# Performance work log

Hardware: AMD Instinct MI355X
Metric: run time of the kernel (lower is better)

## Reference

```python
import jax, jax.numpy as jnp
import numpy as np

DIM = 1024
N_HEADS = 16
HEAD_DIM = DIM // N_HEADS
SCALE = HEAD_DIM ** -0.5


def setup_inputs() -> dict:
    key = jax.random.key(0)
    ks = jax.random.split(key, 10)
    B, L, L_low = 4, 4096, 1024
    s = DIM ** -0.5
    return {
        "x_broad": jax.random.normal(ks[0], (B, L, DIM), jnp.float32),
        "x_low": jax.random.normal(ks[1], (B, L_low, DIM), jnp.float32),
        "Wq": jax.random.normal(ks[2], (DIM, DIM), jnp.float32) * s,
        "bq": jnp.zeros((DIM,), jnp.float32),
        "Wk": jax.random.normal(ks[3], (DIM, DIM), jnp.float32) * s,
        "bk": jnp.zeros((DIM,), jnp.float32),
        "Wv": jax.random.normal(ks[4], (DIM, DIM), jnp.float32) * s,
        "bv": jnp.zeros((DIM,), jnp.float32),
        "Wo": jax.random.normal(ks[5], (DIM, DIM), jnp.float32) * s,
        "bo": jnp.zeros((DIM,), jnp.float32),
    }


def reference(x_broad, x_low, Wq, bq, Wk, bk, Wv, bv, Wo, bo):
    B, L, D = x_broad.shape
    Ll = x_low.shape[1]
    # projections (torch Linear: x @ W.T + b)
    q = (x_broad @ Wq.T + bq).reshape(B, L, N_HEADS, HEAD_DIM)
    k = (x_low @ Wk.T + bk).reshape(B, Ll, N_HEADS, HEAD_DIM)
    v = (x_low @ Wv.T + bv).reshape(B, Ll, N_HEADS, HEAD_DIM)
    # scores: [B, H, L, L_low]
    attn = jnp.einsum("blhd,bmhd->bhlm", q, k) * SCALE
    attn = jax.nn.softmax(attn, axis=-1)
    out = jnp.einsum("bhlm,bmhd->blhd", attn, v).reshape(B, L, D)
    return out @ Wo.T + bo
```

## Files before the change

kernel.cpp:

```cpp
#include <hip/hip_runtime.h>
#include <hip/hip_bf16.h>

typedef __bf16 bf16;
typedef __bf16 bf16x4 __attribute__((ext_vector_type(4)));
typedef __bf16 bf16x8 __attribute__((ext_vector_type(8)));
typedef float f32x4 __attribute__((ext_vector_type(4)));

#define MFMA16(a, b, c) __builtin_amdgcn_mfma_f32_16x16x32_bf16(a, b, c, 0, 0, 0)

constexpr int DIM = 1024;
constexpr int NH = 16;
constexpr int HD = 64;
constexpr float SCALE = 0.125f;
constexpr float L2E = 1.4426950408889634f;
constexpr float SCL2E = SCALE * L2E;

__device__ __forceinline__ float fast_exp2(float x) {
  float r;
  asm("v_exp_f32 %0, %1" : "=v"(r) : "v"(x));
  return r;
}

__device__ __forceinline__ void gl_lds16(const void* g, void* l) {
  __builtin_amdgcn_global_load_lds((const __attribute__((address_space(1))) void*)g,
                                   (__attribute__((address_space(3))) void*)l, 16, 0, 0);
}

__global__ __launch_bounds__(256) void cvt_f32_bf16(const float* __restrict__ s,
                                                    bf16* __restrict__ d, int n8) {
  const int i = blockIdx.x * 256 + threadIdx.x;
  if (i < n8) {
    const float4 v0 = ((const float4*)s)[i * 2];
    const float4 v1 = ((const float4*)s)[i * 2 + 1];
    bf16x8 o = {(bf16)v0.x, (bf16)v0.y, (bf16)v0.z, (bf16)v0.w,
                (bf16)v1.x, (bf16)v1.y, (bf16)v1.z, (bf16)v1.w};
    ((bf16x8*)d)[i] = o;
  }
}

__global__ __launch_bounds__(256) void cvt_w4(const float* __restrict__ a,
                                              const float* __restrict__ b,
                                              const float* __restrict__ c,
                                              const float* __restrict__ d,
                                              bf16* __restrict__ o) {
  constexpr int N8 = DIM * DIM / 8;
  const int i = blockIdx.x * 256 + threadIdx.x;
  const int g = i >> 17;
  const int j = i & (N8 - 1);
  const float* s = (g == 0) ? a : (g == 1) ? b : (g == 2) ? c : d;
  const float4 v0 = ((const float4*)s)[j * 2];
  const float4 v1 = ((const float4*)s)[j * 2 + 1];
  bf16x8 ov = {(bf16)v0.x, (bf16)v0.y, (bf16)v0.z, (bf16)v0.w,
               (bf16)v1.x, (bf16)v1.y, (bf16)v1.z, (bf16)v1.w};
  ((bf16x8*)o)[i] = ov;
}

template <int OUT_MODE>
__global__ __launch_bounds__(256) void gemm_bf16(const bf16* __restrict__ A,
                                                 const bf16* __restrict__ W,
                                                 const float* __restrict__ bias,
                                                 void* __restrict__ Cptr, int Lq,
                                                 float oscale) {
  __shared__ bf16 As[128 * 64];
  __shared__ bf16 Bs[128 * 64];

  const int bm = blockIdx.x * 128;
  const int bn = blockIdx.y * 128;
  const int tid = threadIdx.x;
  const int w = tid >> 6;
  const int lane = tid & 63;
  const int quad = lane >> 4;
  const int l16 = lane & 15;
  const int wm = (w >> 1) * 64;
  const int wn = (w & 1) * 64;
  const int lr = lane >> 3;
  const int sc8 = (((lane & 7) ^ lr)) << 3;
  const int x7 = l16 & 7;

  size_t aOff[4], bOff[4];
#pragma unroll
  for (int r = 0; r < 4; ++r) {
    const int rowt = (r * 4 + w) * 8 + lr;
    aOff[r] = (size_t)(bm + rowt) * DIM + sc8;
    bOff[r] = (size_t)(bn + rowt) * DIM + sc8;
  }

  f32x4 acc[4][4] = {};

  for (int k0 = 0; k0 < DIM; k0 += 64) {
#pragma unroll
    for (int r = 0; r < 4; ++r) {
      gl_lds16(A + aOff[r] + k0, (char*)As + (r * 4 + w) * 1024);
      gl_lds16(W + bOff[r] + k0, (char*)Bs + (r * 4 + w) * 1024);
    }
    __syncthreads();

#pragma unroll
    for (int s = 0; s < 2; ++s) {
      bf16x8 af[4], bfr[4];
#pragma unroll
      for (int mi = 0; mi < 4; ++mi)
        af[mi] = *(const bf16x8*)((char*)As + (wm + mi * 16 + l16) * 128 +
                                  (((quad + 4 * s) ^ x7) << 4));
#pragma unroll
      for (int ni = 0; ni < 4; ++ni)
        bfr[ni] = *(const bf16x8*)((char*)Bs + (wn + ni * 16 + l16) * 128 +
                                   (((quad + 4 * s) ^ x7) << 4));
#pragma unroll
      for (int mi = 0; mi < 4; ++mi)
#pragma unroll
        for (int ni = 0; ni < 4; ++ni)
          acc[mi][ni] = MFMA16(af[mi], bfr[ni], acc[mi][ni]);
    }
    __syncthreads();
  }

#pragma unroll
  for (int mi = 0; mi < 4; ++mi) {
#pragma unroll
    for (int ni = 0; ni < 4; ++ni) {
      const int col = bn + wn + ni * 16 + l16;
      const float bv = bias[col];
#pragma unroll
      for (int r = 0; r < 4; ++r) {
        const int row = bm + wm + mi * 16 + quad * 4 + r;
        const float val = (acc[mi][ni][r] + bv) * oscale;
        if constexpr (OUT_MODE == 0) {
          ((float*)Cptr)[(size_t)row * DIM + col] = val;
        } else if constexpr (OUT_MODE == 1) {
          const int b = row / Lq;
          const int l = row - b * Lq;
          ((bf16*)Cptr)[((size_t)((b * NH + (col >> 6)) * Lq + l) << 6) + (col & 63)] =
              (bf16)val;
        } else {
          const int b = row >> 10;
          const int kv = row & 1023;
          ((bf16*)Cptr)[(((size_t)(b * NH + (col >> 6)) << 6) + (col & 63)) * 1024 + kv] =
              (bf16)val;
        }
      }
    }
  }
}

template <int OUT_MODE, bool A_BF16>
__global__ __launch_bounds__(256) void gemm_nt(const void* __restrict__ Aptr,
                                               const float* __restrict__ W,
                                               const float* __restrict__ bias,
                                               void* __restrict__ Cptr, int Lq,
                                               float oscale) {
  constexpr int LDT = 72;
  __shared__ bf16 As[128 * LDT];
  __shared__ bf16 Bs[128 * LDT];

  const int bm = blockIdx.x * 128;
  const int bn = blockIdx.y * 128;
  const int tid = threadIdx.x;
  const int w = tid >> 6;
  const int lane = tid & 63;
  const int quad = lane >> 4;
  const int l16 = lane & 15;
  const int wm = (w >> 1) * 64;
  const int wn = (w & 1) * 64;

  f32x4 acc[4][4] = {};

  for (int k0 = 0; k0 < DIM; k0 += 64) {
#pragma unroll
    for (int i = 0; i < 8; ++i) {
      int f = i * 256 + tid;
      int row = f >> 4;
      int c4 = (f & 15) << 2;
      const float4 v = *(const float4*)(W + (size_t)(bn + row) * DIM + k0 + c4);
      bf16x4 bv = {(bf16)v.x, (bf16)v.y, (bf16)v.z, (bf16)v.w};
      *(bf16x4*)&Bs[row * LDT + c4] = bv;
    }
    if constexpr (A_BF16) {
      const bf16* Ab = (const bf16*)Aptr;
#pragma unroll
      for (int i = 0; i < 4; ++i) {
        int f = i * 256 + tid;
        int row = f >> 3;
        int c8 = (f & 7) << 3;
        *(bf16x8*)&As[row * LDT + c8] =
            *(const bf16x8*)(Ab + (size_t)(bm + row) * DIM + k0 + c8);
      }
    } else {
      const float* Af = (const float*)Aptr;
#pragma unroll
      for (int i = 0; i < 8; ++i) {
        int f = i * 256 + tid;
        int row = f >> 4;
        int c4 = (f & 15) << 2;
        const float4 v = *(const float4*)(Af + (size_t)(bm + row) * DIM + k0 + c4);
        bf16x4 av = {(bf16)v.x, (bf16)v.y, (bf16)v.z, (bf16)v.w};
        *(bf16x4*)&As[row * LDT + c4] = av;
      }
    }
    __syncthreads();

#pragma unroll
    for (int sub = 0; sub < 2; ++sub) {
      bf16x8 af[4], bfr[4];
#pragma unroll
      for (int mi = 0; mi < 4; ++mi)
        af[mi] = *(const bf16x8*)&As[(wm + mi * 16 + l16) * LDT + sub * 32 + quad * 8];
#pragma unroll
      for (int ni = 0; ni < 4; ++ni)
        bfr[ni] = *(const bf16x8*)&Bs[(wn + ni * 16 + l16) * LDT + sub * 32 + quad * 8];
#pragma unroll
      for (int mi = 0; mi < 4; ++mi)
#pragma unroll
        for (int ni = 0; ni < 4; ++ni)
          acc[mi][ni] = MFMA16(af[mi], bfr[ni], acc[mi][ni]);
    }
    __syncthreads();
  }

#pragma unroll
  for (int mi = 0; mi < 4; ++mi) {
#pragma unroll
    for (int ni = 0; ni < 4; ++ni) {
      const int col = bn + wn + ni * 16 + l16;
      const float bv = bias[col];
#pragma unroll
      for (int r = 0; r < 4; ++r) {
        const int row = bm + wm + mi * 16 + quad * 4 + r;
        const float val = (acc[mi][ni][r] + bv) * oscale;
        if constexpr (OUT_MODE == 0) {
          ((float*)Cptr)[(size_t)row * DIM + col] = val;
        } else if constexpr (OUT_MODE == 1) {
          const int b = row / Lq;
          const int l = row - b * Lq;
          ((bf16*)Cptr)[((size_t)((b * NH + (col >> 6)) * Lq + l) << 6) + (col & 63)] =
              (bf16)val;
        } else {
          const int b = row >> 10;
          const int kv = row & 1023;
          ((bf16*)Cptr)[(((size_t)(b * NH + (col >> 6)) << 6) + (col & 63)) * 1024 + kv] =
              (bf16)val;
        }
      }
    }
  }
}

__global__ __launch_bounds__(256) void attn_fused(const bf16* __restrict__ Q,
                                                  const bf16* __restrict__ K,
                                                  const bf16* __restrict__ VT,
                                                  bf16* __restrict__ O) {
  __shared__ bf16 Ks[2][64 * 64];
  __shared__ bf16 Vs[2][64 * 64];
  __shared__ bf16 Ps[4 * 16 * 64];

  const int qt = blockIdx.x;
  const int h = blockIdx.y;
  const int b = blockIdx.z;
  const int tid = threadIdx.x;
  const int w = tid >> 6;
  const int lane = tid & 63;
  const int quad = lane >> 4;
  const int l16 = lane & 15;
  const int lr = lane >> 3;
  const int sc8 = (((lane & 7) ^ lr)) << 3;
  const int x7 = l16 & 7;

  const bf16* Qp = Q + ((size_t)(b * NH + h) * 4096 + qt * 128 + w * 32 + l16) * HD + quad * 8;
  const bf16* Kb = K + (size_t)(b * NH + h) * 1024 * HD;
  const bf16* Vb = VT + (size_t)(b * NH + h) * HD * 1024;

  bf16x8 qf[2][2];
#pragma unroll
  for (int g = 0; g < 2; ++g)
#pragma unroll
    for (int s = 0; s < 2; ++s) qf[g][s] = *(const bf16x8*)(Qp + g * 16 * HD + s * 32);

  char* pw = (char*)&Ps[w * 16 * 64];

  f32x4 oacc[2][4] = {};
  f32x4 lacc[2] = {};

  bf16x8 ones;
#pragma unroll
  for (int i = 0; i < 8; ++i) ones[i] = (bf16)1.0f;

  auto stage = [&](int kt, int bi) {
#pragma unroll
    for (int c2 = 0; c2 < 2; ++c2) {
      const int c = c2 * 4 + w;
      gl_lds16(Kb + (size_t)(kt + c * 8 + lr) * HD + sc8, (char*)&Ks[bi][0] + c * 1024);
      gl_lds16(Vb + (size_t)(c * 8 + lr) * 1024 + kt + sc8, (char*)&Vs[bi][0] + c * 1024);
    }
  };

  stage(0, 0);
  int buf = 0;
  for (int kt = 0; kt < 1024; kt += 64) {
    __syncthreads();
    if (kt + 64 < 1024) stage(kt + 64, buf ^ 1);

    bf16x8 kf[4][2];
#pragma unroll
    for (int nt = 0; nt < 4; ++nt)
#pragma unroll
      for (int s = 0; s < 2; ++s)
        kf[nt][s] = *(const bf16x8*)((char*)&Ks[buf][0] + (nt * 16 + l16) * 128 +
                                     (((quad + 4 * s) ^ x7) << 4));

    bf16x8 pf[2][2];
#pragma unroll
    for (int g = 0; g < 2; ++g) {
      __builtin_amdgcn_s_setprio(1);
#pragma unroll
      for (int nt = 0; nt < 4; ++nt) {
        f32x4 a = {0.f, 0.f, 0.f, 0.f};
        a = MFMA16(kf[nt][0], qf[g][0], a);
        a = MFMA16(kf[nt][1], qf[g][1], a);
        bf16x4 pb;
#pragma unroll
        for (int r = 0; r < 4; ++r) pb[r] = (bf16)fast_exp2(a[r]);
        *(bf16x4*)(pw + l16 * 128 + ((nt * 32 + quad * 8) ^ (x7 << 4))) = pb;
      }
      __builtin_amdgcn_s_setprio(0);
#pragma unroll
      for (int s = 0; s < 2; ++s)
        pf[g][s] = *(const bf16x8*)(pw + l16 * 128 + ((s * 64 + quad * 16) ^ (x7 << 4)));
      lacc[g] = MFMA16(ones, pf[g][0], lacc[g]);
      lacc[g] = MFMA16(ones, pf[g][1], lacc[g]);
    }

    __builtin_amdgcn_s_setprio(1);
#pragma unroll
    for (int dt = 0; dt < 4; ++dt) {
      bf16x8 vf0 = *(const bf16x8*)((char*)&Vs[buf][0] + (dt * 16 + l16) * 128 +
                                    ((quad ^ x7) << 4));
      bf16x8 vf1 = *(const bf16x8*)((char*)&Vs[buf][0] + (dt * 16 + l16) * 128 +
                                    ((((quad + 4)) ^ x7) << 4));
      oacc[0][dt] = MFMA16(vf0, pf[0][0], oacc[0][dt]);
      oacc[0][dt] = MFMA16(vf1, pf[0][1], oacc[0][dt]);
      oacc[1][dt] = MFMA16(vf0, pf[1][0], oacc[1][dt]);
      oacc[1][dt] = MFMA16(vf1, pf[1][1], oacc[1][dt]);
    }
    __builtin_amdgcn_s_setprio(0);
    buf ^= 1;
  }

  const float inv[2] = {1.f / lacc[0][0], 1.f / lacc[1][0]};

#pragma unroll
  for (int g = 0; g < 2; ++g) {
    const size_t orow =
        ((size_t)(b * 4096 + qt * 128 + w * 32 + g * 16 + l16)) * DIM + h * 64;
#pragma unroll
    for (int dt = 0; dt < 4; ++dt) {
      bf16x4 ov = {(bf16)(oacc[g][dt][0] * inv[g]), (bf16)(oacc[g][dt][1] * inv[g]),
                   (bf16)(oacc[g][dt][2] * inv[g]), (bf16)(oacc[g][dt][3] * inv[g])};
      *(bf16x4*)(O + orow + dt * 16 + quad * 4) = ov;
    }
  }
}

extern "C" void kernel_launch(void* const* d_in, const int* in_sizes, int n_in,
                              void* d_out, int out_size, void* d_ws, size_t ws_size,
                              hipStream_t stream) {
  const float* x_broad = (const float*)d_in[0];
  const float* x_low = (const float*)d_in[1];
  const float* Wq = (const float*)d_in[2];
  const float* bq = (const float*)d_in[3];
  const float* Wk = (const float*)d_in[4];
  const float* bk = (const float*)d_in[5];
  const float* Wv = (const float*)d_in[6];
  const float* bv = (const float*)d_in[7];
  const float* Wo = (const float*)d_in[8];
  const float* bo = (const float*)d_in[9];

  constexpr int B = 4, L = 4096, LL = 1024;
  const size_t qBytes = (size_t)B * NH * L * HD * 2;
  const size_t kvBytes = (size_t)B * NH * LL * HD * 2;
  const size_t oBytes = qBytes;
  const size_t xlBytes = kvBytes;
  const size_t wBytes = (size_t)DIM * DIM * 2;

  char* ws = (char*)d_ws;
  bf16* Qw = (bf16*)ws;
  bf16* Kw = (bf16*)(ws + qBytes);
  bf16* Vw = (bf16*)(ws + qBytes + kvBytes);
  bf16* Ow = (bf16*)(ws + qBytes + 2 * kvBytes);

  const dim3 blk(256);
  const size_t need = qBytes + 2 * kvBytes + oBytes + xlBytes + 4 * wBytes;

  if (ws_size >= need) {
    bf16* xbB = Ow;
    bf16* xlB = (bf16*)(ws + qBytes + 2 * kvBytes + oBytes);
    bf16* WqB = (bf16*)(ws + qBytes + 2 * kvBytes + oBytes + xlBytes);
    bf16* WkB = WqB + (size_t)DIM * DIM;
    bf16* WvB = WkB + (size_t)DIM * DIM;
    bf16* WoB = WvB + (size_t)DIM * DIM;

    hipLaunchKernelGGL(cvt_f32_bf16, dim3(B * L * DIM / 8 / 256), blk, 0, stream,
                       x_broad, xbB, B * L * DIM / 8);
    hipLaunchKernelGGL(cvt_f32_bf16, dim3(B * LL * DIM / 8 / 256), blk, 0, stream,
                       x_low, xlB, B * LL * DIM / 8);
    hipLaunchKernelGGL(cvt_w4, dim3(4 * DIM * DIM / 8 / 256), blk, 0, stream, Wq, Wk,
                       Wv, Wo, WqB);

    hipLaunchKernelGGL((gemm_bf16<1>), dim3(B * L / 128, DIM / 128), blk, 0, stream,
                       xbB, WqB, bq, Qw, L, SCL2E);
    hipLaunchKernelGGL((gemm_bf16<1>), dim3(B * LL / 128, DIM / 128), blk, 0, stream,
                       xlB, WkB, bk, Kw, LL, 1.0f);
    hipLaunchKernelGGL((gemm_bf16<2>), dim3(B * LL / 128, DIM / 128), blk, 0, stream,
                       xlB, WvB, bv, Vw, LL, 1.0f);
    hipLaunchKernelGGL(attn_fused, dim3(L / 128, NH, B), blk, 0, stream, Qw, Kw, Vw, Ow);
    hipLaunchKernelGGL((gemm_bf16<0>), dim3(B * L / 128, DIM / 128), blk, 0, stream,
                       Ow, WoB, bo, d_out, 1, 1.0f);
  } else {
    hipLaunchKernelGGL((gemm_nt<1, false>), dim3(B * L / 128, DIM / 128), blk, 0,
                       stream, x_broad, Wq, bq, Qw, L, SCL2E);
    hipLaunchKernelGGL((gemm_nt<1, false>), dim3(B * LL / 128, DIM / 128), blk, 0,
                       stream, x_low, Wk, bk, Kw, LL, 1.0f);
    hipLaunchKernelGGL((gemm_nt<2, false>), dim3(B * LL / 128, DIM / 128), blk, 0,
                       stream, x_low, Wv, bv, Vw, LL, 1.0f);
    hipLaunchKernelGGL(attn_fused, dim3(L / 128, NH, B), blk, 0, stream, Qw, Kw, Vw, Ow);
    hipLaunchKernelGGL((gemm_nt<0, true>), dim3(B * L / 128, DIM / 128), blk, 0,
                       stream, Ow, Wo, bo, d_out, 1, 1.0f);
  }
}
```

Measured before the change: 372.5 us.

## Double attention query tile per block and compute V projection transposed

The attention kernel now handles 256 query rows per block (64 per wave, four 16-row groups), so each staged K/V tile is reused across twice as many queries and the grid is halved. The V projection is recomputed as Wv·x_low^T with swapped operands (OUT_MODE 3, per-row bias), so the transposed V layout is written with contiguous kv stores instead of strided scatter. This costs more accumulator registers per wave (lower occupancy possible) and fewer blocks in the attention grid.

```diff
diff --git a/kernel.cpp b/kernel.cpp
--- a/kernel.cpp
+++ b/kernel.cpp
@@ -106,6 +106,109 @@
       for (int ni = 0; ni < 4; ++ni)
         bfr[ni] = *(const bf16x8*)((char*)Bs + (wn + ni * 16 + l16) * 128 +
                                    (((quad + 4 * s) ^ x7) << 4));
+#pragma unroll
+      for (int mi = 0; mi < 4; ++mi)
+#pragma unroll
+        for (int ni = 0; ni < 4; ++ni)
+          acc[mi][ni] = MFMA16(af[mi], bfr[ni], acc[mi][ni]);
+    }
+    __syncthreads();
+  }
+
+#pragma unroll
+  for (int mi = 0; mi < 4; ++mi) {
+#pragma unroll
+    for (int ni = 0; ni < 4; ++ni) {
+      const int col = bn + wn + ni * 16 + l16;
+      const float bv = (OUT_MODE == 3) ? 0.f : bias[col];
+#pragma unroll
+      for (int r = 0; r < 4; ++r) {
+        const int row = bm + wm + mi * 16 + quad * 4 + r;
+        if constexpr (OUT_MODE == 0) {
+          const float val = (acc[mi][ni][r] + bv) * oscale;
+          ((float*)Cptr)[(size_t)row * DIM + col] = val;
+        } else if constexpr (OUT_MODE == 1) {
+          const float val = (acc[mi][ni][r] + bv) * oscale;
+          const int b = row / Lq;
+          const int l = row - b * Lq;
+          ((bf16*)Cptr)[((size_t)((b * NH + (col >> 6)) * Lq + l) << 6) + (col & 63)] =
+              (bf16)val;
+        } else {
+          const float val = acc[mi][ni][r] + bias[row];
+          const int bb = col >> 10;
+          const int kv = col & 1023;
+          ((bf16*)Cptr)[((size_t)(bb * 1024 + row)) * 1024 + kv] = (bf16)val;
+        }
+      }
+    }
+  }
+}
+
+template <int OUT_MODE, bool A_BF16>
+__global__ __launch_bounds__(256) void gemm_nt(const void* __restrict__ Aptr,
+                                               const float* __restrict__ W,
+                                               const float* __restrict__ bias,
+                                               void* __restrict__ Cptr, int Lq,
+                                               float oscale) {
+  constexpr int LDT = 72;
+  __shared__ bf16 As[128 * LDT];
+  __shared__ bf16 Bs[128 * LDT];
+
+  const int bm = blockIdx.x * 128;
+  const int bn = blockIdx.y * 128;
+  const int tid = threadIdx.x;
+  const int w = tid >> 6;
+  const int lane = tid & 63;
+  const int quad = lane >> 4;
+  const int l16 = lane & 15;
+  const int wm = (w >> 1) * 64;
+  const int wn = (w & 1) * 64;
+
+  f32x4 acc[4][4] = {};
+
+  for (int k0 = 0; k0 < DIM; k0 += 64) {
+#pragma unroll
+    for (int i = 0; i < 8; ++i) {
+      int f = i * 256 + tid;
+      int row = f >> 4;
+      int c4 = (f & 15) << 2;
+      const float4 v = *(const float4*)(W + (size_t)(bn + row) * DIM + k0 + c4);
+      bf16x4 bv = {(bf16)v.x, (bf16)v.y, (bf16)v.z, (bf16)v.w};
+      *(bf16x4*)&Bs[row * LDT + c4] = bv;
+    }
+    if constexpr (A_BF16) {
+      const bf16* Ab = (const bf16*)Aptr;
+#pragma unroll
+      for (int i = 0; i < 4; ++i) {
+        int f = i * 256 + tid;
+        int row = f >> 3;
+        int c8 = (f & 7) << 3;
+        *(bf16x8*)&As[row * LDT + c8] =
+            *(const bf16x8*)(Ab + (size_t)(bm + row) * DIM + k0 + c8);
+      }
+    } else {
+      const float* Af = (const float*)Aptr;
+#pragma unroll
+      for (int i = 0; i < 8; ++i) {
+        int f = i * 256 + tid;
+        int row = f >> 4;
+        int c4 = (f & 15) << 2;
+        const float4 v = *(const float4*)(Af + (size_t)(bm + row) * DIM + k0 + c4);
+        bf16x4 av = {(bf16)v.x, (bf16)v.y, (bf16)v.z, (bf16)v.w};
+        *(bf16x4*)&As[row * LDT + c4] = av;
+      }
+    }
+    __syncthreads();
+
+#pragma unroll
+    for (int sub = 0; sub < 2; ++sub) {
+      bf16x8 af[4], bfr[4];
+#pragma unroll
+      for (int mi = 0; mi < 4; ++mi)
+        af[mi] = *(const bf16x8*)&As[(wm + mi * 16 + l16) * LDT + sub * 32 + quad * 8];
+#pragma unroll
+      for (int ni = 0; ni < 4; ++ni)
+        bfr[ni] = *(const bf16x8*)&Bs[(wn + ni * 16 + l16) * LDT + sub * 32 + quad * 8];
 #pragma unroll
       for (int mi = 0; mi < 4; ++mi)
 #pragma unroll
@@ -143,108 +246,6 @@
   }
 }
 
-template <int OUT_MODE, bool A_BF16>
-__global__ __launch_bounds__(256) void gemm_nt(const void* __restrict__ Aptr,
-                                               const float* __restrict__ W,
-                                               const float* __restrict__ bias,
-                                               void* __restrict__ Cptr, int Lq,
-                                               float oscale) {
-  constexpr int LDT = 72;
-  __shared__ bf16 As[128 * LDT];
-  __shared__ bf16 Bs[128 * LDT];
-
-  const int bm = blockIdx.x * 128;
-  const int bn = blockIdx.y * 128;
-  const int tid = threadIdx.x;
-  const int w = tid >> 6;
-  const int lane = tid & 63;
-  const int quad = lane >> 4;
-  const int l16 = lane & 15;
-  const int wm = (w >> 1) * 64;
-  const int wn = (w & 1) * 64;
-
-  f32x4 acc[4][4] = {};
-
-  for (int k0 = 0; k0 < DIM; k0 += 64) {
-#pragma unroll
-    for (int i = 0; i < 8; ++i) {
-      int f = i * 256 + tid;
-      int row = f >> 4;
-      int c4 = (f & 15) << 2;
-      const float4 v = *(const float4*)(W + (size_t)(bn + row) * DIM + k0 + c4);
-      bf16x4 bv = {(bf16)v.x, (bf16)v.y, (bf16)v.z, (bf16)v.w};
-      *(bf16x4*)&Bs[row * LDT + c4] = bv;
-    }
-    if constexpr (A_BF16) {
-      const bf16* Ab = (const bf16*)Aptr;
-#pragma unroll
-      for (int i = 0; i < 4; ++i) {
-        int f = i * 256 + tid;
-        int row = f >> 3;
-        int c8 = (f & 7) << 3;
-        *(bf16x8*)&As[row * LDT + c8] =
-            *(const bf16x8*)(Ab + (size_t)(bm + row) * DIM + k0 + c8);
-      }
-    } else {
-      const float* Af = (const float*)Aptr;
-#pragma unroll
-      for (int i = 0; i < 8; ++i) {
-        int f = i * 256 + tid;
-        int row = f >> 4;
-        int c4 = (f & 15) << 2;
-        const float4 v = *(const float4*)(Af + (size_t)(bm + row) * DIM + k0 + c4);
-        bf16x4 av = {(bf16)v.x, (bf16)v.y, (bf16)v.z, (bf16)v.w};
-        *(bf16x4*)&As[row * LDT + c4] = av;
-      }
-    }
-    __syncthreads();
-
-#pragma unroll
-    for (int sub = 0; sub < 2; ++sub) {
-      bf16x8 af[4], bfr[4];
-#pragma unroll
-      for (int mi = 0; mi < 4; ++mi)
-        af[mi] = *(const bf16x8*)&As[(wm + mi * 16 + l16) * LDT + sub * 32 + quad * 8];
-#pragma unroll
-      for (int ni = 0; ni < 4; ++ni)
-        bfr[ni] = *(const bf16x8*)&Bs[(wn + ni * 16 + l16) * LDT + sub * 32 + quad * 8];
-#pragma unroll
-      for (int mi = 0; mi < 4; ++mi)
-#pragma unroll
-        for (int ni = 0; ni < 4; ++ni)
-          acc[mi][ni] = MFMA16(af[mi], bfr[ni], acc[mi][ni]);
-    }
-    __syncthreads();
-  }
-
-#pragma unroll
-  for (int mi = 0; mi < 4; ++mi) {
-#pragma unroll
-    for (int ni = 0; ni < 4; ++ni) {
-      const int col = bn + wn + ni * 16 + l16;
-      const float bv = bias[col];
-#pragma unroll
-      for (int r = 0; r < 4; ++r) {
-        const int row = bm + wm + mi * 16 + quad * 4 + r;
-        const float val = (acc[mi][ni][r] + bv) * oscale;
-        if constexpr (OUT_MODE == 0) {
-          ((float*)Cptr)[(size_t)row * DIM + col] = val;
-        } else if constexpr (OUT_MODE == 1) {
-          const int b = row / Lq;
-          const int l = row - b * Lq;
-          ((bf16*)Cptr)[((size_t)((b * NH + (col >> 6)) * Lq + l) << 6) + (col & 63)] =
-              (bf16)val;
-        } else {
-          const int b = row >> 10;
-          const int kv = row & 1023;
-          ((bf16*)Cptr)[(((size_t)(b * NH + (col >> 6)) << 6) + (col & 63)) * 1024 + kv] =
-              (bf16)val;
-        }
-      }
-    }
-  }
-}
-
 __global__ __launch_bounds__(256) void attn_fused(const bf16* __restrict__ Q,
                                                   const bf16* __restrict__ K,
                                                   const bf16* __restrict__ VT,
@@ -265,20 +266,21 @@
   const int sc8 = (((lane & 7) ^ lr)) << 3;
   const int x7 = l16 & 7;
 
-  const bf16* Qp = Q + ((size_t)(b * NH + h) * 4096 + qt * 128 + w * 32 + l16) * HD + quad * 8;
+  const bf16* Qp =
+      Q + ((size_t)(b * NH + h) * 4096 + qt * 256 + w * 64 + l16) * HD + quad * 8;
   const bf16* Kb = K + (size_t)(b * NH + h) * 1024 * HD;
   const bf16* Vb = VT + (size_t)(b * NH + h) * HD * 1024;
 
-  bf16x8 qf[2][2];
-#pragma unroll
-  for (int g = 0; g < 2; ++g)
+  bf16x8 qf[4][2];
+#pragma unroll
+  for (int g = 0; g < 4; ++g)
 #pragma unroll
     for (int s = 0; s < 2; ++s) qf[g][s] = *(const bf16x8*)(Qp + g * 16 * HD + s * 32);
 
   char* pw = (char*)&Ps[w * 16 * 64];
 
-  f32x4 oacc[2][4] = {};
-  f32x4 lacc[2] = {};
+  f32x4 oacc[4][4] = {};
+  f32x4 lacc[4] = {};
 
   bf16x8 ones;
 #pragma unroll
@@ -307,9 +309,9 @@
         kf[nt][s] = *(const bf16x8*)((char*)&Ks[buf][0] + (nt * 16 + l16) * 128 +
                                      (((quad + 4 * s) ^ x7) << 4));
 
-    bf16x8 pf[2][2];
-#pragma unroll
-    for (int g = 0; g < 2; ++g) {
+    bf16x8 pf[4][2];
+#pragma unroll
+    for (int g = 0; g < 4; ++g) {
       __builtin_amdgcn_s_setprio(1);
 #pragma unroll
       for (int nt = 0; nt < 4; ++nt) {
@@ -336,25 +338,25 @@
                                     ((quad ^ x7) << 4));
       bf16x8 vf1 = *(const bf16x8*)((char*)&Vs[buf][0] + (dt * 16 + l16) * 128 +
                                     ((((quad + 4)) ^ x7) << 4));
-      oacc[0][dt] = MFMA16(vf0, pf[0][0], oacc[0][dt]);
-      oacc[0][dt] = MFMA16(vf1, pf[0][1], oacc[0][dt]);
-      oacc[1][dt] = MFMA16(vf0, pf[1][0], oacc[1][dt]);
-      oacc[1][dt] = MFMA16(vf1, pf[1][1], oacc[1][dt]);
+#pragma unroll
+      for (int g = 0; g < 4; ++g) {
+        oacc[g][dt] = MFMA16(vf0, pf[g][0], oacc[g][dt]);
+        oacc[g][dt] = MFMA16(vf1, pf[g][1], oacc[g][dt]);
+      }
     }
     __builtin_amdgcn_s_setprio(0);
     buf ^= 1;
   }
 
-  const float inv[2] = {1.f / lacc[0][0], 1.f / lacc[1][0]};
-
-#pragma unroll
-  for (int g = 0; g < 2; ++g) {
+#pragma unroll
+  for (int g = 0; g < 4; ++g) {
+    const float inv = 1.f / lacc[g][0];
     const size_t orow =
-        ((size_t)(b * 4096 + qt * 128 + w * 32 + g * 16 + l16)) * DIM + h * 64;
+        ((size_t)(b * 4096 + qt * 256 + w * 64 + g * 16 + l16)) * DIM + h * 64;
 #pragma unroll
     for (int dt = 0; dt < 4; ++dt) {
-      bf16x4 ov = {(bf16)(oacc[g][dt][0] * inv[g]), (bf16)(oacc[g][dt][1] * inv[g]),
-                   (bf16)(oacc[g][dt][2] * inv[g]), (bf16)(oacc[g][dt][3] * inv[g])};
+      bf16x4 ov = {(bf16)(oacc[g][dt][0] * inv), (bf16)(oacc[g][dt][1] * inv),
+                   (bf16)(oacc[g][dt][2] * inv), (bf16)(oacc[g][dt][3] * inv)};
       *(bf16x4*)(O + orow + dt * 16 + quad * 4) = ov;
     }
   }
@@ -409,9 +411,9 @@
                        xbB, WqB, bq, Qw, L, SCL2E);
     hipLaunchKernelGGL((gemm_bf16<1>), dim3(B * LL / 128, DIM / 128), blk, 0, stream,
                        xlB, WkB, bk, Kw, LL, 1.0f);
-    hipLaunchKernelGGL((gemm_bf16<2>), dim3(B * LL / 128, DIM / 128), blk, 0, stream,
-                       xlB, WvB, bv, Vw, LL, 1.0f);
-    hipLaunchKernelGGL(attn_fused, dim3(L / 128, NH, B), blk, 0, stream, Qw, Kw, Vw, Ow);
+    hipLaunchKernelGGL((gemm_bf16<3>), dim3(DIM / 128, B * LL / 128), blk, 0, stream,
+                       WvB, xlB, bv, Vw, LL, 1.0f);
+    hipLaunchKernelGGL(attn_fused, dim3(L / 256, NH, B), blk, 0, stream, Qw, Kw, Vw, Ow);
     hipLaunchKernelGGL((gemm_bf16<0>), dim3(B * L / 128, DIM / 128), blk, 0, stream,
                        Ow, WoB, bo, d_out, 1, 1.0f);
   } else {
@@ -421,7 +423,7 @@
                        stream, x_low, Wk, bk, Kw, LL, 1.0f);
     hipLaunchKernelGGL((gemm_nt<2, false>), dim3(B * LL / 128, DIM / 128), blk, 0,
                        stream, x_low, Wv, bv, Vw, LL, 1.0f);
-    hipLaunchKernelGGL(attn_fused, dim3(L / 128, NH, B), blk, 0, stream, Qw, Kw, Vw, Ow);
+    hipLaunchKernelGGL(attn_fused, dim3(L / 256, NH, B), blk, 0, stream, Qw, Kw, Vw, Ow);
     hipLaunchKernelGGL((gemm_nt<0, true>), dim3(B * L / 128, DIM / 128), blk, 0,
                        stream, Ow, Wo, bo, d_out, 1, 1.0f);
   }
```

After: 375.8 us. No clear change (+0.9%).
